# Kernel optimization log

Measured on AMD Instinct MI355X. Metric: run time of the kernel, lower is better.

## Reference

```python
import jax, jax.numpy as jnp
import numpy as np
import math

D_PAIR, D_BIAS, H, DH = 128, 128, 4, 32
B, L = 1, 384


def setup_inputs() -> dict:
    key = jax.random.key(0)
    ks = jax.random.split(key, 12)
    s = 0.02
    return {
        "pair": jax.random.normal(ks[0], (B, L, L, D_PAIR), jnp.float32),
        "bias": jax.random.normal(ks[1], (B, L, L, D_BIAS), jnp.float32),
        "ln_g": jnp.ones((D_PAIR,), jnp.float32),
        "ln_b": jnp.zeros((D_PAIR,), jnp.float32),
        "Wq": jax.random.normal(ks[2], (D_PAIR, H * DH), jnp.float32) * s,
        "Wk": jax.random.normal(ks[3], (D_PAIR, H * DH), jnp.float32) * s,
        "Wv": jax.random.normal(ks[4], (D_PAIR, H * DH), jnp.float32) * s,
        "Wb": jax.random.normal(ks[5], (D_BIAS, H), jnp.float32) * s,
        "Wg": jax.random.normal(ks[6], (D_PAIR, H * DH), jnp.float32) * s,
        "bg": jnp.ones((H * DH,), jnp.float32),
        "Wo": jax.random.normal(ks[7], (H * DH, D_PAIR), jnp.float32) * s,
        "bo": jnp.zeros((D_PAIR,), jnp.float32),
    }


def reference(pair, bias, ln_g, ln_b, Wq, Wk, Wv, Wb, Wg, bg, Wo, bo):
    # is_row=True: attend along the first L axis by permuting (i<->n)
    b_, l_ = pair.shape[:2]
    p = jnp.transpose(pair, (0, 2, 1, 3))  # [B,L,L,Dp]
    # LayerNorm over last dim (eps matches torch default)
    mu = jnp.mean(p, axis=-1, keepdims=True)
    var = jnp.mean(jnp.square(p - mu), axis=-1, keepdims=True)
    p = (p - mu) / jnp.sqrt(var + 1e-5) * ln_g + ln_b

    scaling = 1.0 / math.sqrt(DH)
    q = (p @ Wq).reshape(b_, l_, l_, H, DH) * scaling          # [B,n,i,h,c]
    k = (p @ Wk).reshape(b_, l_, l_, H, DH) / math.sqrt(l_)    # [B,n,j,h,c]
    # tied axial attention logits: sum over the n axis + projected bias
    logits = jnp.einsum("bnihc,bnjhc->bijh", q, k) + bias @ Wb  # [B,L,L,h]
    attn = jax.nn.softmax(logits, axis=-2)                      # softmax over j

    v = (p @ Wv).reshape(b_, l_, l_, H, DH)                     # [B,k,j,h,d]
    g = jax.nn.sigmoid(p @ Wg + bg)                             # [B,L,L,h*d]
    o = jnp.einsum("bijh,bkjhd->bikhd", attn, v).reshape(b_, l_, l_, H * DH)
    out = (g * o) @ Wo + bo                                     # [B,L,L,Dp]
    return jnp.transpose(out, (0, 2, 1, 3))  # undo is_row permute
```

## Files before the change

kernel.cpp:

```cpp
#include <hip/hip_runtime.h>
#include <math.h>

typedef unsigned short us;
typedef unsigned long long u64;
typedef short bf16x8 __attribute__((ext_vector_type(8)));
typedef short bf16x4 __attribute__((ext_vector_type(4)));
typedef float f32x4 __attribute__((ext_vector_type(4)));

#define LQ 384
#define DPAIR 128
#define KDIM 12288

#define WT_OFF   0UL
#define P_OFF    262144UL
#define LOG_OFF  262144UL
#define ATT_OFF  2621440UL
#define Q_OFF    38010880UL
#define K_OFF    75759616UL
#define V_OFF    113508352UL
#define G_OFF    151257088UL

__device__ __forceinline__ us f2bf(float x){
  unsigned u = __builtin_bit_cast(unsigned, x);
  return (us)((u + 0x7FFFu + ((u >> 16) & 1u)) >> 16);
}
__device__ __forceinline__ float bf2f(us b){
  unsigned u = ((unsigned)b) << 16;
  return __builtin_bit_cast(float, u);
}
__device__ __forceinline__ void gl_lds16(const void* g, void* l){
  __builtin_amdgcn_global_load_lds((const __attribute__((address_space(1))) unsigned*)g,
                                   (__attribute__((address_space(3))) unsigned*)l, 16, 0, 0);
}
__device__ __forceinline__ float wsum(float x){
  #pragma unroll
  for (int o = 32; o; o >>= 1) x += __shfl_xor(x, o, 64);
  return x;
}
__device__ __forceinline__ float wmaxr(float x){
  #pragma unroll
  for (int o = 32; o; o >>= 1) x = fmaxf(x, __shfl_xor(x, o, 64));
  return x;
}
__device__ __forceinline__ void stage_pair(const us* __restrict__ Arow, const us* __restrict__ Brow,
                                           size_t strideA, size_t strideB, int koff,
                                           us* ldsA, us* ldsB, int tid)
{
  #pragma unroll
  for (int s = 0; s < 4; ++s) {
    int slot = s * 256 + tid;
    int rrow = slot >> 3, cc = slot & 7;
    int cg = cc ^ (rrow & 7);
    gl_lds16(Arow + (size_t)rrow * strideA + koff + cg * 8, &ldsA[slot * 8]);
    gl_lds16(Brow + (size_t)rrow * strideB + koff + cg * 8, &ldsB[slot * 8]);
  }
}

__global__ __launch_bounds__(256) void k_pack(
    const float* __restrict__ Wq, const float* __restrict__ Wk,
    const float* __restrict__ Wv, const float* __restrict__ Wg,
    const float* __restrict__ Wo, us* __restrict__ wt)
{
  int idx = blockIdx.x * 256 + threadIdx.x;
  int m = idx >> 14, rr = idx & 16383, k = rr >> 7, n = rr & 127;
  const float* W; float s;
  switch (m) {
    case 0: W = Wq; s = 0.17677669529663687f; break;
    case 1: W = Wk; s = 0.05103103630798287f; break;
    case 2: W = Wv; s = 1.f; break;
    case 3: W = Wg; s = 1.f; break;
    default: W = Wo; s = 1.f; break;
  }
  wt[m * 16384 + n * 128 + k] = f2bf(W[k * 128 + n] * s);
}

__global__ __launch_bounds__(256) void k_ln(
    const float* __restrict__ pair, const float* __restrict__ lng,
    const float* __restrict__ lnb, us* __restrict__ P)
{
  const int tid = threadIdx.x, w = tid >> 6, l = tid & 63;
  const int gw = blockIdx.x * 4 + w;
  const int b = gw / 12, a0 = (gw % 12) * 32;
  const float2 lg = ((const float2*)lng)[l];
  const float2 lb = ((const float2*)lnb)[l];
  for (int it = 0; it < 8; ++it) {
    float2 x[4];
    #pragma unroll
    for (int rr = 0; rr < 4; ++rr) {
      int a = a0 + it * 4 + rr;
      x[rr] = ((const float2*)(pair + ((size_t)b * LQ + a) * DPAIR))[l];
    }
    #pragma unroll
    for (int rr = 0; rr < 4; ++rr) {
      int a = a0 + it * 4 + rr;
      float s = wsum(x[rr].x + x[rr].y);
      float q = wsum(x[rr].x * x[rr].x + x[rr].y * x[rr].y);
      float mu = s * (1.f / 128.f);
      float var = q * (1.f / 128.f) - mu * mu;
      float rstd = rsqrtf(var + 1e-5f);
      float y0 = (x[rr].x - mu) * rstd * lg.x + lb.x;
      float y1 = (x[rr].y - mu) * rstd * lg.y + lb.y;
      unsigned pk = (unsigned)f2bf(y0) | ((unsigned)f2bf(y1) << 16);
      ((unsigned*)(P + ((size_t)a * LQ + b) * DPAIR))[l] = pk;
    }
  }
}

__global__ __launch_bounds__(256, 4) void k_qkvg(
    const us* __restrict__ P, const us* __restrict__ wt,
    const float* __restrict__ bgp,
    us* __restrict__ Qw, us* __restrict__ Kw, us* __restrict__ Vw, us* __restrict__ Gw)
{
  __shared__ __attribute__((aligned(16))) us lds[17408];
  const int tid = threadIdx.x, w = tid >> 6, l = tid & 63;
  const int bx = blockIdx.x;
  const int xg = bx & 7, u = bx >> 3;
  int type, a_base, b0; bool qk;
  if (u < 288) {
    type = u & 1;
    int tq = xg * 144 + (u >> 1);
    a_base = (tq / 12) * 4; b0 = (tq % 12) * 32; qk = true;
  } else {
    int v = u - 288;
    type = 2 + (v & 1);
    int tv = xg * 144 + (v >> 1);
    a_base = tv / 3; b0 = (tv % 3) * 128; qk = false;
  }
  const us* W = wt + type * 16384;
  const int m0 = (w & 1) * 64, n0 = (w >> 1) * 64;
  const int row16 = l & 15, kq = l >> 4;

  #pragma unroll
  for (int s = 0; s < 8; ++s) {
    int slot = s * 256 + tid;
    int r = slot >> 4, c = slot & 15;
    int cg = (c & 8) | ((c & 7) ^ (r & 7));
    size_t prow = qk ? ((size_t)(a_base + (r >> 5)) * LQ + b0 + (r & 31))
                     : ((size_t)a_base * LQ + b0 + r);
    gl_lds16(P + prow * DPAIR + cg * 8, &lds[slot * 8]);
  }
  f32x4 acc[4][4];
  #pragma unroll
  for (int mt = 0; mt < 4; ++mt)
    #pragma unroll
    for (int nt = 0; nt < 4; ++nt) acc[mt][nt] = (f32x4){0.f, 0.f, 0.f, 0.f};
  asm volatile("s_waitcnt vmcnt(0)" ::: "memory");
  __syncthreads();

  #pragma unroll
  for (int kb = 0; kb < 4; ++kb) {
    bf16x8 bv[4], af[4];
    #pragma unroll
    for (int nt = 0; nt < 4; ++nt)
      bv[nt] = *(const bf16x8*)&W[(n0 + nt * 16 + row16) * DPAIR + kb * 32 + kq * 8];
    #pragma unroll
    for (int mt = 0; mt < 4; ++mt) {
      int r = m0 + mt * 16 + row16;
      int c = kb * 4 + kq;
      int cg = (c & 8) | ((c & 7) ^ (r & 7));
      af[mt] = *(const bf16x8*)&lds[r * 128 + cg * 8];
    }
    #pragma unroll
    for (int mt = 0; mt < 4; ++mt)
      #pragma unroll
      for (int nt = 0; nt < 4; ++nt)
        acc[mt][nt] = __builtin_amdgcn_mfma_f32_16x16x32_bf16(af[mt], bv[nt], acc[mt][nt], 0, 0, 0);
  }
  __syncthreads();

  if (qk) {
    us* T = lds;
    #pragma unroll
    for (int nt = 0; nt < 4; ++nt) {
      int n = n0 + nt * 16 + row16, h = n >> 5, cc = n & 31;
      #pragma unroll
      for (int mt = 0; mt < 4; ++mt) {
        f32x4 vv = acc[mt][nt];
        #pragma unroll
        for (int v4 = 0; v4 < 4; ++v4) {
          int r = m0 + mt * 16 + kq * 4 + v4;
          T[(h * 32 + (r & 31)) * 132 + (r >> 5) * 32 + cc] = f2bf(vv[v4]);
        }
      }
    }
    __syncthreads();
    us* dst = (type == 0) ? Qw : Kw;
    #pragma unroll
    for (int it = 0; it < 8; ++it) {
      int slot = it * 256 + tid;
      int combo = slot >> 4, chunk = slot & 15;
      int h = combo >> 5, bl = combo & 31;
      bf16x8 val = *(const bf16x8*)&T[combo * 132 + chunk * 8];
      *(bf16x8*)&dst[((size_t)h * LQ + b0 + bl) * KDIM + a_base * 32 + chunk * 8] = val;
    }
  } else if (type == 2) {
    us* T = lds;
    #pragma unroll
    for (int nt = 0; nt < 4; ++nt) {
      int col = n0 + nt * 16 + row16;
      #pragma unroll
      for (int mt = 0; mt < 4; ++mt) {
        int rowb = m0 + mt * 16 + kq * 4;
        f32x4 vv = acc[mt][nt];
        *(unsigned*)&T[col * 132 + rowb]     = (unsigned)f2bf(vv[0]) | ((unsigned)f2bf(vv[1]) << 16);
        *(unsigned*)&T[col * 132 + rowb + 2] = (unsigned)f2bf(vv[2]) | ((unsigned)f2bf(vv[3]) << 16);
      }
    }
    __syncthreads();
    #pragma unroll
    for (int it = 0; it < 8; ++it) {
      int slot = tid + 256 * it;
      int d = slot >> 4, jc = slot & 15;
      bf16x4 lo = *(const bf16x4*)&T[d * 132 + jc * 8];
      bf16x4 hi = *(const bf16x4*)&T[d * 132 + jc * 8 + 4];
      bf16x8 val = __builtin_shufflevector(lo, hi, 0, 1, 2, 3, 4, 5, 6, 7);
      int h = d >> 5, dd = d & 31;
      *(bf16x8*)&Vw[((size_t)h * KDIM + a_base * 32 + dd) * LQ + b0 + jc * 8] = val;
    }
  } else {
    us* Cs = lds;
    #pragma unroll
    for (int nt = 0; nt < 4; ++nt) {
      int col = n0 + nt * 16 + row16;
      float bgv = bgp[col];
      #pragma unroll
      for (int mt = 0; mt < 4; ++mt) {
        f32x4 vv = acc[mt][nt];
        #pragma unroll
        for (int v4 = 0; v4 < 4; ++v4) {
          float e = __expf(-(vv[v4] + bgv));
          Cs[(m0 + mt * 16 + kq * 4 + v4) * 136 + col] = f2bf(1.f / (1.f + e));
        }
      }
    }
    __syncthreads();
    #pragma unroll
    for (int it = 0; it < 8; ++it) {
      int slot = tid + 256 * it;
      int row = slot >> 4, chunk = slot & 15;
      bf16x8 val = *(const bf16x8*)&Cs[row * 136 + chunk * 8];
      *(bf16x8*)&Gw[((size_t)(a_base * LQ + b0 + row)) * DPAIR + chunk * 8] = val;
    }
  }
}

__global__ __launch_bounds__(256) void k_biasproj(
    const float* __restrict__ bias, const float* __restrict__ Wb,
    float* __restrict__ logits)
{
  __shared__ float bps[128][5];
  const int tid = threadIdx.x, w = tid >> 6, l = tid & 63;
  const int i = blockIdx.x / 3, j0 = (blockIdx.x % 3) * 128;
  const int g = l >> 4, sl = l & 15;
  const float4* Wb4 = (const float4*)Wb;
  float4 wb[8];
  #pragma unroll
  for (int e = 0; e < 8; ++e) wb[e] = Wb4[sl * 8 + e];
  for (int it = 0; it < 8; ++it) {
    int j = j0 + w * 32 + it * 4 + g;
    const float4* br = (const float4*)(bias + ((size_t)i * LQ + j) * DPAIR);
    float4 xa = br[sl * 2], xb = br[sl * 2 + 1];
    float p0 = 0.f, p1 = 0.f, p2 = 0.f, p3 = 0.f;
    #pragma unroll
    for (int e = 0; e < 4; ++e) {
      float xe = ((const float*)&xa)[e];
      p0 += xe * wb[e].x; p1 += xe * wb[e].y; p2 += xe * wb[e].z; p3 += xe * wb[e].w;
      float xf = ((const float*)&xb)[e];
      p0 += xf * wb[4 + e].x; p1 += xf * wb[4 + e].y; p2 += xf * wb[4 + e].z; p3 += xf * wb[4 + e].w;
    }
    #pragma unroll
    for (int o = 1; o < 16; o <<= 1) {
      p0 += __shfl_xor(p0, o, 64);
      p1 += __shfl_xor(p1, o, 64);
      p2 += __shfl_xor(p2, o, 64);
      p3 += __shfl_xor(p3, o, 64);
    }
    if (sl == 0) {
      int row = w * 32 + it * 4 + g;
      bps[row][0] = p0; bps[row][1] = p1; bps[row][2] = p2; bps[row][3] = p3;
    }
  }
  __syncthreads();
  #pragma unroll
  for (int rep = 0; rep < 2; ++rep) {
    int slot = rep * 256 + tid;
    int h = slot >> 7, jj = slot & 127;
    logits[((size_t)h * LQ + i) * LQ + j0 + jj] = bps[jj][h];
  }
}

__global__ __launch_bounds__(256) void k_logits(
    const us* __restrict__ Qw, const us* __restrict__ Kw, float* __restrict__ logits)
{
  __shared__ __attribute__((aligned(16))) us AB[2][2][8192];
  const int tid = threadIdx.x, w = tid >> 6, l = tid & 63;
  const int bx = blockIdx.x;
  const int xg = bx & 7, yg = bx >> 3;
  const int set = xg * 24 + yg / 3, j0 = (yg % 3) * 128;
  const int h = set / 48, rem = set % 48, i0 = (rem / 16) * 128, ks = rem % 16;
  const us* Ab = Qw + (size_t)h * LQ * KDIM + (size_t)i0 * KDIM;
  const us* Bb = Kw + (size_t)h * LQ * KDIM + (size_t)j0 * KDIM;
  f32x4 acc[4][4];
  #pragma unroll
  for (int mt = 0; mt < 4; ++mt)
    #pragma unroll
    for (int nt = 0; nt < 4; ++nt) acc[mt][nt] = (f32x4){0.f, 0.f, 0.f, 0.f};
  const int m0 = (w & 1) * 64, n0 = (w >> 1) * 64;
  const int row16 = l & 15, kq = l >> 4;
  stage_pair(Ab, Bb, KDIM, KDIM, ks * 768, AB[0][0], AB[0][1], tid);
  for (int kk = 0; kk < 12; ++kk) {
    const int cur = kk & 1;
    if (kk < 11) {
      stage_pair(Ab, Bb, KDIM, KDIM, ks * 768 + (kk + 1) * 64, AB[cur ^ 1][0], AB[cur ^ 1][1], tid);
      asm volatile("s_waitcnt vmcnt(8)" ::: "memory");
    } else {
      asm volatile("s_waitcnt vmcnt(0)" ::: "memory");
    }
    __syncthreads();
    #pragma unroll
    for (int kb = 0; kb < 2; ++kb) {
      bf16x8 af[4], bv[4];
      #pragma unroll
      for (int mt = 0; mt < 4; ++mt) {
        int r = m0 + mt * 16 + row16;
        int c = (kb * 4 + kq) ^ (r & 7);
        af[mt] = *(const bf16x8*)&AB[cur][0][r * 64 + c * 8];
      }
      #pragma unroll
      for (int nt = 0; nt < 4; ++nt) {
        int r = n0 + nt * 16 + row16;
        int c = (kb * 4 + kq) ^ (r & 7);
        bv[nt] = *(const bf16x8*)&AB[cur][1][r * 64 + c * 8];
      }
      #pragma unroll
      for (int mt = 0; mt < 4; ++mt)
        #pragma unroll
        for (int nt = 0; nt < 4; ++nt)
          acc[mt][nt] = __builtin_amdgcn_mfma_f32_16x16x32_bf16(af[mt], bv[nt], acc[mt][nt], 0, 0, 0);
    }
    __syncthreads();
  }
  #pragma unroll
  for (int mt = 0; mt < 4; ++mt)
    #pragma unroll
    for (int nt = 0; nt < 4; ++nt)
      #pragma unroll
      for (int v4 = 0; v4 < 4; ++v4) {
        int i = i0 + m0 + mt * 16 + kq * 4 + v4;
        int j = j0 + n0 + nt * 16 + row16;
        atomicAdd(&logits[((size_t)h * LQ + i) * LQ + j], acc[mt][nt][v4]);
      }
}

__global__ __launch_bounds__(256) void k_softmax(
    const float* __restrict__ logits, us* __restrict__ attn)
{
  const int tid = threadIdx.x, h = tid >> 6, l = tid & 63;
  const int i = blockIdx.x;
  const float* lrow = logits + ((size_t)h * LQ + i) * LQ;
  float x[6];
  #pragma unroll
  for (int s = 0; s < 6; ++s) x[s] = lrow[l + 64 * s];
  float mx = x[0];
  #pragma unroll
  for (int s = 1; s < 6; ++s) mx = fmaxf(mx, x[s]);
  mx = wmaxr(mx);
  float e[6], sum = 0.f;
  #pragma unroll
  for (int s = 0; s < 6; ++s) { e[s] = expf(x[s] - mx); sum += e[s]; }
  sum = wsum(sum);
  float rinv = 1.f / sum;
  #pragma unroll
  for (int s = 0; s < 6; ++s)
    attn[((size_t)h * LQ + i) * LQ + l + 64 * s] = f2bf(e[s] * rinv);
}

__global__ __launch_bounds__(256) void k_ogemm(
    const us* __restrict__ attn, const us* __restrict__ Vw, us* __restrict__ Gw)
{
  __shared__ __attribute__((aligned(16))) us AB[2][2][8192];
  const int tid = threadIdx.x, w = tid >> 6, l = tid & 63;
  const int bx = blockIdx.x;
  const int xg = bx & 7, yg = bx >> 3;
  const int set = xg * 48 + yg / 3, i0 = (yg % 3) * 128;
  const int h = set / 96, n0 = (set % 96) * 128;
  const us* Ab = attn + (size_t)h * LQ * LQ + (size_t)i0 * LQ;
  const us* Bb = Vw + (size_t)h * KDIM * LQ + (size_t)n0 * LQ;
  f32x4 acc[4][4];
  #pragma unroll
  for (int mt = 0; mt < 4; ++mt)
    #pragma unroll
    for (int nt = 0; nt < 4; ++nt) acc[mt][nt] = (f32x4){0.f, 0.f, 0.f, 0.f};
  const int m0 = (w & 1) * 64, n0w = (w >> 1) * 64;
  const int row16 = l & 15, kq = l >> 4;
  stage_pair(Ab, Bb, LQ, LQ, 0, AB[0][0], AB[0][1], tid);
  for (int kk = 0; kk < 6; ++kk) {
    const int cur = kk & 1;
    if (kk < 5) {
      stage_pair(Ab, Bb, LQ, LQ, (kk + 1) * 64, AB[cur ^ 1][0], AB[cur ^ 1][1], tid);
      asm volatile("s_waitcnt vmcnt(8)" ::: "memory");
    } else {
      asm volatile("s_waitcnt vmcnt(0)" ::: "memory");
    }
    __syncthreads();
    #pragma unroll
    for (int kb = 0; kb < 2; ++kb) {
      bf16x8 af[4], bv[4];
      #pragma unroll
      for (int mt = 0; mt < 4; ++mt) {
        int r = m0 + mt * 16 + row16;
        int c = (kb * 4 + kq) ^ (r & 7);
        af[mt] = *(const bf16x8*)&AB[cur][0][r * 64 + c * 8];
      }
      #pragma unroll
      for (int nt = 0; nt < 4; ++nt) {
        int r = n0w + nt * 16 + row16;
        int c = (kb * 4 + kq) ^ (r & 7);
        bv[nt] = *(const bf16x8*)&AB[cur][1][r * 64 + c * 8];
      }
      #pragma unroll
      for (int mt = 0; mt < 4; ++mt)
        #pragma unroll
        for (int nt = 0; nt < 4; ++nt)
          acc[mt][nt] = __builtin_amdgcn_mfma_f32_16x16x32_bf16(af[mt], bv[nt], acc[mt][nt], 0, 0, 0);
    }
    __syncthreads();
  }
  us* C = (us*)AB;
  #pragma unroll
  for (int mt = 0; mt < 4; ++mt)
    #pragma unroll
    for (int nt = 0; nt < 4; ++nt)
      #pragma unroll
      for (int v4 = 0; v4 < 4; ++v4)
        C[(m0 + mt * 16 + kq * 4 + v4) * 128 + n0w + nt * 16 + row16] = f2bf(acc[mt][nt][v4]);
  __syncthreads();
  const int k0 = n0 >> 5;
  #pragma unroll
  for (int it = 0; it < 8; ++it) {
    int slot = tid + 256 * it;
    int xr = slot >> 4, ch = slot & 15;
    bf16x8 ov = *(const bf16x8*)&C[xr * 128 + ch * 8];
    size_t eaddr = ((size_t)(i0 + xr) * LQ + k0 + (ch >> 2)) * DPAIR + h * 32 + (ch & 3) * 8;
    bf16x8 gv = *(const bf16x8*)&Gw[eaddr];
    bf16x8 ev;
    #pragma unroll
    for (int q = 0; q < 8; ++q)
      ev[q] = (short)f2bf(bf2f((us)(unsigned short)ov[q]) * bf2f((us)(unsigned short)gv[q]));
    *(bf16x8*)&Gw[eaddr] = ev;
  }
}

__global__ __launch_bounds__(256) void k_final(
    const us* __restrict__ E, const us* __restrict__ wt,
    const float* __restrict__ bo, float* __restrict__ out)
{
  __shared__ __attribute__((aligned(16))) us A[128 * 128];
  const int tid = threadIdx.x, w = tid >> 6, l = tid & 63;
  const int y = blockIdx.x / 3, x0 = (blockIdx.x % 3) * 128;
  #pragma unroll
  for (int s4 = 0; s4 < 8; ++s4) {
    int slot = s4 * 256 + tid;
    int r = slot >> 4, c = slot & 15;
    int cg = (c & 8) | ((c & 7) ^ (r & 7));
    gl_lds16(E + ((size_t)(x0 + r) * LQ + y) * DPAIR + cg * 8, &A[slot * 8]);
  }
  asm volatile("s_waitcnt vmcnt(0)" ::: "memory");
  __syncthreads();
  const us* W = wt + 4 * 16384;
  const int m0 = (w & 1) * 64, n0w = (w >> 1) * 64;
  const int row16 = l & 15, kq = l >> 4;
  f32x4 acc[4][4];
  #pragma unroll
  for (int mt = 0; mt < 4; ++mt)
    #pragma unroll
    for (int nt = 0; nt < 4; ++nt) acc[mt][nt] = (f32x4){0.f, 0.f, 0.f, 0.f};
  #pragma unroll
  for (int kb = 0; kb < 4; ++kb) {
    bf16x8 af[4], bv[4];
    #pragma unroll
    for (int mt = 0; mt < 4; ++mt) {
      int r = m0 + mt * 16 + row16;
      int c = (kb * 4 + kq);
      int cg = (c & 8) | ((c & 7) ^ (r & 7));
      af[mt] = *(const bf16x8*)&A[r * 128 + cg * 8];
    }
    #pragma unroll
    for (int nt = 0; nt < 4; ++nt)
      bv[nt] = *(const bf16x8*)&W[(n0w + nt * 16 + row16) * 128 + kb * 32 + kq * 8];
    #pragma unroll
    for (int mt = 0; mt < 4; ++mt)
      #pragma unroll
      for (int nt = 0; nt < 4; ++nt)
        acc[mt][nt] = __builtin_amdgcn_mfma_f32_16x16x32_bf16(af[mt], bv[nt], acc[mt][nt], 0, 0, 0);
  }
  #pragma unroll
  for (int nt = 0; nt < 4; ++nt) {
    int n = n0w + nt * 16 + row16;
    float bov = bo[n];
    #pragma unroll
    for (int mt = 0; mt < 4; ++mt)
      #pragma unroll
      for (int v4 = 0; v4 < 4; ++v4) {
        int m = m0 + mt * 16 + kq * 4 + v4;
        out[((size_t)y * LQ + x0 + m) * DPAIR + n] = acc[mt][nt][v4] + bov;
      }
  }
}

extern "C" void kernel_launch(void* const* d_in, const int* in_sizes, int n_in,
                              void* d_out, int out_size, void* d_ws, size_t ws_size,
                              hipStream_t stream)
{
  const float* pair = (const float*)d_in[0];
  const float* bias = (const float*)d_in[1];
  const float* lng  = (const float*)d_in[2];
  const float* lnb  = (const float*)d_in[3];
  const float* Wq   = (const float*)d_in[4];
  const float* Wk   = (const float*)d_in[5];
  const float* Wv   = (const float*)d_in[6];
  const float* Wb   = (const float*)d_in[7];
  const float* Wg   = (const float*)d_in[8];
  const float* bg   = (const float*)d_in[9];
  const float* Wo   = (const float*)d_in[10];
  const float* bo   = (const float*)d_in[11];

  char* ws = (char*)d_ws;
  us* wt     = (us*)(ws + WT_OFF);
  us* P      = (us*)(ws + P_OFF);
  us* Qw     = (us*)(ws + Q_OFF);
  us* Kw     = (us*)(ws + K_OFF);
  us* Vw     = (us*)(ws + V_OFF);
  us* Gw     = (us*)(ws + G_OFF);
  us* attn   = (us*)(ws + ATT_OFF);
  float* logits = (float*)(ws + LOG_OFF);

  k_pack<<<320, 256, 0, stream>>>(Wq, Wk, Wv, Wg, Wo, wt);
  k_ln<<<1152, 256, 0, stream>>>(pair, lng, lnb, P);
  k_qkvg<<<4608, 256, 0, stream>>>(P, wt, bg, Qw, Kw, Vw, Gw);
  k_biasproj<<<1152, 256, 0, stream>>>(bias, Wb, logits);
  k_logits<<<576, 256, 0, stream>>>(Qw, Kw, logits);
  k_softmax<<<384, 256, 0, stream>>>(logits, attn);
  k_ogemm<<<1152, 256, 0, stream>>>(attn, Vw, Gw);
  k_final<<<1152, 256, 0, stream>>>(Gw, wt, bo, (float*)d_out);
}
```

Before: 256.4 us.

## Fuse prep kernels, merge bias projection into logits, add nontemporal and staged stores

Merges weight packing with LayerNorm into one launch, and folds the bias projection into the logits kernel as extra blocks that atomically add into a memset-zeroed logits buffer. Q/K/V/G writes become nontemporal stores. The final GEMM output is staged through LDS so fp32 rows are written as coalesced 16-byte nontemporal stores. Fewer launch gaps and better store efficiency are traded for an extra memset, more atomics on logits, and larger LDS in the final kernel.

```diff
diff --git a/kernel.cpp b/kernel.cpp
--- a/kernel.cpp
+++ b/kernel.cpp
@@ -32,6 +32,9 @@
   __builtin_amdgcn_global_load_lds((const __attribute__((address_space(1))) unsigned*)g,
                                    (__attribute__((address_space(3))) unsigned*)l, 16, 0, 0);
 }
+__device__ __forceinline__ void nt_st8(us* p, bf16x8 v){
+  __builtin_nontemporal_store(v, (bf16x8*)p);
+}
 __device__ __forceinline__ float wsum(float x){
   #pragma unroll
   for (int o = 32; o; o >>= 1) x += __shfl_xor(x, o, 64);
@@ -56,30 +59,30 @@
   }
 }
 
-__global__ __launch_bounds__(256) void k_pack(
+__global__ __launch_bounds__(256) void k_prep(
     const float* __restrict__ Wq, const float* __restrict__ Wk,
     const float* __restrict__ Wv, const float* __restrict__ Wg,
-    const float* __restrict__ Wo, us* __restrict__ wt)
-{
-  int idx = blockIdx.x * 256 + threadIdx.x;
-  int m = idx >> 14, rr = idx & 16383, k = rr >> 7, n = rr & 127;
-  const float* W; float s;
-  switch (m) {
-    case 0: W = Wq; s = 0.17677669529663687f; break;
-    case 1: W = Wk; s = 0.05103103630798287f; break;
-    case 2: W = Wv; s = 1.f; break;
-    case 3: W = Wg; s = 1.f; break;
-    default: W = Wo; s = 1.f; break;
-  }
-  wt[m * 16384 + n * 128 + k] = f2bf(W[k * 128 + n] * s);
-}
-
-__global__ __launch_bounds__(256) void k_ln(
+    const float* __restrict__ Wo, us* __restrict__ wt,
     const float* __restrict__ pair, const float* __restrict__ lng,
     const float* __restrict__ lnb, us* __restrict__ P)
 {
+  const int bx = blockIdx.x;
+  if (bx < 320) {
+    int idx = bx * 256 + threadIdx.x;
+    int m = idx >> 14, rr = idx & 16383, k = rr >> 7, n = rr & 127;
+    const float* W; float s;
+    switch (m) {
+      case 0: W = Wq; s = 0.17677669529663687f; break;
+      case 1: W = Wk; s = 0.05103103630798287f; break;
+      case 2: W = Wv; s = 1.f; break;
+      case 3: W = Wg; s = 1.f; break;
+      default: W = Wo; s = 1.f; break;
+    }
+    wt[m * 16384 + n * 128 + k] = f2bf(W[k * 128 + n] * s);
+    return;
+  }
   const int tid = threadIdx.x, w = tid >> 6, l = tid & 63;
-  const int gw = blockIdx.x * 4 + w;
+  const int gw = (bx - 320) * 4 + w;
   const int b = gw / 12, a0 = (gw % 12) * 32;
   const float2 lg = ((const float2*)lng)[l];
   const float2 lb = ((const float2*)lnb)[l];
@@ -191,7 +194,7 @@
       int combo = slot >> 4, chunk = slot & 15;
       int h = combo >> 5, bl = combo & 31;
       bf16x8 val = *(const bf16x8*)&T[combo * 132 + chunk * 8];
-      *(bf16x8*)&dst[((size_t)h * LQ + b0 + bl) * KDIM + a_base * 32 + chunk * 8] = val;
+      nt_st8(&dst[((size_t)h * LQ + b0 + bl) * KDIM + a_base * 32 + chunk * 8], val);
     }
   } else if (type == 2) {
     us* T = lds;
@@ -215,7 +218,7 @@
       bf16x4 hi = *(const bf16x4*)&T[d * 132 + jc * 8 + 4];
       bf16x8 val = __builtin_shufflevector(lo, hi, 0, 1, 2, 3, 4, 5, 6, 7);
       int h = d >> 5, dd = d & 31;
-      *(bf16x8*)&Vw[((size_t)h * KDIM + a_base * 32 + dd) * LQ + b0 + jc * 8] = val;
+      nt_st8(&Vw[((size_t)h * KDIM + a_base * 32 + dd) * LQ + b0 + jc * 8], val);
     }
   } else {
     us* Cs = lds;
@@ -239,62 +242,61 @@
       int slot = tid + 256 * it;
       int row = slot >> 4, chunk = slot & 15;
       bf16x8 val = *(const bf16x8*)&Cs[row * 136 + chunk * 8];
-      *(bf16x8*)&Gw[((size_t)(a_base * LQ + b0 + row)) * DPAIR + chunk * 8] = val;
-    }
-  }
-}
-
-__global__ __launch_bounds__(256) void k_biasproj(
+      nt_st8(&Gw[((size_t)(a_base * LQ + b0 + row)) * DPAIR + chunk * 8], val);
+    }
+  }
+}
+
+__global__ __launch_bounds__(256) void k_logits2(
+    const us* __restrict__ Qw, const us* __restrict__ Kw,
     const float* __restrict__ bias, const float* __restrict__ Wb,
     float* __restrict__ logits)
-{
-  __shared__ float bps[128][5];
-  const int tid = threadIdx.x, w = tid >> 6, l = tid & 63;
-  const int i = blockIdx.x / 3, j0 = (blockIdx.x % 3) * 128;
-  const int g = l >> 4, sl = l & 15;
-  const float4* Wb4 = (const float4*)Wb;
-  float4 wb[8];
-  #pragma unroll
-  for (int e = 0; e < 8; ++e) wb[e] = Wb4[sl * 8 + e];
-  for (int it = 0; it < 8; ++it) {
-    int j = j0 + w * 32 + it * 4 + g;
-    const float4* br = (const float4*)(bias + ((size_t)i * LQ + j) * DPAIR);
-    float4 xa = br[sl * 2], xb = br[sl * 2 + 1];
-    float p0 = 0.f, p1 = 0.f, p2 = 0.f, p3 = 0.f;
-    #pragma unroll
-    for (int e = 0; e < 4; ++e) {
-      float xe = ((const float*)&xa)[e];
-      p0 += xe * wb[e].x; p1 += xe * wb[e].y; p2 += xe * wb[e].z; p3 += xe * wb[e].w;
-      float xf = ((const float*)&xb)[e];
-      p0 += xf * wb[4 + e].x; p1 += xf * wb[4 + e].y; p2 += xf * wb[4 + e].z; p3 += xf * wb[4 + e].w;
-    }
-    #pragma unroll
-    for (int o = 1; o < 16; o <<= 1) {
-      p0 += __shfl_xor(p0, o, 64);
-      p1 += __shfl_xor(p1, o, 64);
-      p2 += __shfl_xor(p2, o, 64);
-      p3 += __shfl_xor(p3, o, 64);
-    }
-    if (sl == 0) {
-      int row = w * 32 + it * 4 + g;
-      bps[row][0] = p0; bps[row][1] = p1; bps[row][2] = p2; bps[row][3] = p3;
-    }
-  }
-  __syncthreads();
-  #pragma unroll
-  for (int rep = 0; rep < 2; ++rep) {
-    int slot = rep * 256 + tid;
-    int h = slot >> 7, jj = slot & 127;
-    logits[((size_t)h * LQ + i) * LQ + j0 + jj] = bps[jj][h];
-  }
-}
-
-__global__ __launch_bounds__(256) void k_logits(
-    const us* __restrict__ Qw, const us* __restrict__ Kw, float* __restrict__ logits)
 {
   __shared__ __attribute__((aligned(16))) us AB[2][2][8192];
   const int tid = threadIdx.x, w = tid >> 6, l = tid & 63;
   const int bx = blockIdx.x;
+  if (bx >= 576) {
+    float* bps = (float*)AB;
+    const int u2 = bx - 576;
+    const int i = u2 / 3, j0 = (u2 % 3) * 128;
+    const int g = l >> 4, sl = l & 15;
+    const float4* Wb4 = (const float4*)Wb;
+    float4 wb[8];
+    #pragma unroll
+    for (int e = 0; e < 8; ++e) wb[e] = Wb4[sl * 8 + e];
+    for (int it = 0; it < 8; ++it) {
+      int j = j0 + w * 32 + it * 4 + g;
+      const float4* br = (const float4*)(bias + ((size_t)i * LQ + j) * DPAIR);
+      float4 xa = br[sl * 2], xb = br[sl * 2 + 1];
+      float p0 = 0.f, p1 = 0.f, p2 = 0.f, p3 = 0.f;
+      #pragma unroll
+      for (int e = 0; e < 4; ++e) {
+        float xe = ((const float*)&xa)[e];
+        p0 += xe * wb[e].x; p1 += xe * wb[e].y; p2 += xe * wb[e].z; p3 += xe * wb[e].w;
+        float xf = ((const float*)&xb)[e];
+        p0 += xf * wb[4 + e].x; p1 += xf * wb[4 + e].y; p2 += xf * wb[4 + e].z; p3 += xf * wb[4 + e].w;
+      }
+      #pragma unroll
+      for (int o = 1; o < 16; o <<= 1) {
+        p0 += __shfl_xor(p0, o, 64);
+        p1 += __shfl_xor(p1, o, 64);
+        p2 += __shfl_xor(p2, o, 64);
+        p3 += __shfl_xor(p3, o, 64);
+      }
+      if (sl == 0) {
+        int row = w * 32 + it * 4 + g;
+        bps[row * 5 + 0] = p0; bps[row * 5 + 1] = p1; bps[row * 5 + 2] = p2; bps[row * 5 + 3] = p3;
+      }
+    }
+    __syncthreads();
+    #pragma unroll
+    for (int rep = 0; rep < 2; ++rep) {
+      int slot = rep * 256 + tid;
+      int h = slot >> 7, jj = slot & 127;
+      atomicAdd(&logits[((size_t)h * LQ + i) * LQ + j0 + jj], bps[jj * 5 + h]);
+    }
+    return;
+  }
   const int xg = bx & 7, yg = bx >> 3;
   const int set = xg * 24 + yg / 3, j0 = (yg % 3) * 128;
   const int h = set / 48, rem = set % 48, i0 = (rem / 16) * 128, ks = rem % 16;
@@ -455,7 +457,7 @@
     const us* __restrict__ E, const us* __restrict__ wt,
     const float* __restrict__ bo, float* __restrict__ out)
 {
-  __shared__ __attribute__((aligned(16))) us A[128 * 128];
+  __shared__ __attribute__((aligned(16))) us A[17408];
   const int tid = threadIdx.x, w = tid >> 6, l = tid & 63;
   const int y = blockIdx.x / 3, x0 = (blockIdx.x % 3) * 128;
   #pragma unroll
@@ -494,17 +496,34 @@
       for (int nt = 0; nt < 4; ++nt)
         acc[mt][nt] = __builtin_amdgcn_mfma_f32_16x16x32_bf16(af[mt], bv[nt], acc[mt][nt], 0, 0, 0);
   }
-  #pragma unroll
-  for (int nt = 0; nt < 4; ++nt) {
-    int n = n0w + nt * 16 + row16;
-    float bov = bo[n];
-    #pragma unroll
-    for (int mt = 0; mt < 4; ++mt)
-      #pragma unroll
-      for (int v4 = 0; v4 < 4; ++v4) {
-        int m = m0 + mt * 16 + kq * 4 + v4;
-        out[((size_t)y * LQ + x0 + m) * DPAIR + n] = acc[mt][nt][v4] + bov;
-      }
+  __syncthreads();
+  float* Sf = (float*)A;
+  #pragma unroll
+  for (int half = 0; half < 2; ++half) {
+    if ((w & 1) == half) {
+      #pragma unroll
+      for (int nt = 0; nt < 4; ++nt) {
+        int col = n0w + nt * 16 + row16;
+        float bov = bo[col];
+        #pragma unroll
+        for (int mt = 0; mt < 4; ++mt) {
+          f32x4 vv = acc[mt][nt];
+          #pragma unroll
+          for (int v4 = 0; v4 < 4; ++v4)
+            Sf[(mt * 16 + kq * 4 + v4) * 136 + col] = vv[v4] + bov;
+        }
+      }
+    }
+    __syncthreads();
+    #pragma unroll
+    for (int it = 0; it < 8; ++it) {
+      int slot = it * 256 + tid;
+      int rw = slot >> 5, ch = slot & 31;
+      f32x4 v = *(const f32x4*)&Sf[rw * 136 + ch * 4];
+      __builtin_nontemporal_store(v,
+        (f32x4*)&out[((size_t)y * LQ + x0 + half * 64 + rw) * DPAIR + ch * 4]);
+    }
+    __syncthreads();
   }
 }
 
@@ -535,11 +554,10 @@
   us* attn   = (us*)(ws + ATT_OFF);
   float* logits = (float*)(ws + LOG_OFF);
 
-  k_pack<<<320, 256, 0, stream>>>(Wq, Wk, Wv, Wg, Wo, wt);
-  k_ln<<<1152, 256, 0, stream>>>(pair, lng, lnb, P);
+  k_prep<<<1472, 256, 0, stream>>>(Wq, Wk, Wv, Wg, Wo, wt, pair, lng, lnb, P);
   k_qkvg<<<4608, 256, 0, stream>>>(P, wt, bg, Qw, Kw, Vw, Gw);
-  k_biasproj<<<1152, 256, 0, stream>>>(bias, Wb, logits);
-  k_logits<<<576, 256, 0, stream>>>(Qw, Kw, logits);
+  (void)hipMemsetAsync(logits, 0, (size_t)4 * LQ * LQ * 4, stream);
+  k_logits2<<<1728, 256, 0, stream>>>(Qw, Kw, bias, Wb, logits);
   k_softmax<<<384, 256, 0, stream>>>(logits, attn);
   k_ogemm<<<1152, 256, 0, stream>>>(attn, Vw, Gw);
   k_final<<<1152, 256, 0, stream>>>(Gw, wt, bo, (float*)d_out);
```

New measurement: 246.6 us. -3.8%, faster.
